# Performance work log

Measured on AMD Instinct MI355X. Metric: run time of the kernel, lower is better.

## Reference

```python
import jax, jax.numpy as jnp
import numpy as np

S = 7
B = 2
CLS = 20
N = CLS + B * 5  # 30
LAMBDA_COORD = 5.0
LAMBDA_NOOBJ = 0.5
BATCH = 16384


def setup_inputs() -> dict:
    key = jax.random.key(0)
    k1, k2, k3 = jax.random.split(key, 3)
    pred = jax.random.uniform(k1, (BATCH, S, S, N), dtype=jnp.float32)
    target = jax.random.uniform(k2, (BATCH, S, S, N), dtype=jnp.float32)
    # conf channel (index 4) must be exactly 0 or 1 -- it drives the obj/noobj masks
    obj = (jax.random.uniform(k3, (BATCH, S, S)) < 0.15).astype(jnp.float32)
    target = target.at[..., 4].set(obj)
    return {"pred": pred, "target": target}


def _iou(b1, b2):
    # b1: [M, B, 4] xyxy, b2: [M, 4] xyxy -> [M, B]
    lt = jnp.maximum(b1[..., :2], b2[:, None, :2])
    rb = jnp.minimum(b1[..., 2:], b2[:, None, 2:])
    wh = jnp.clip(rb - lt, 0.0)
    inter = wh[..., 0] * wh[..., 1]
    area1 = (b1[..., 2] - b1[..., 0]) * (b1[..., 3] - b1[..., 1])
    area2 = ((b2[:, 2] - b2[:, 0]) * (b2[:, 3] - b2[:, 1]))[:, None]
    union = area1 + area2 - inter
    return jnp.where(union > 0, inter / union, 0.0)


def reference(pred, target):
    batch = pred.shape[0]
    p = pred.reshape(-1, N)   # [M, 30], M = batch*S*S
    t = target.reshape(-1, N)
    obj = (t[:, 4] == 1).astype(pred.dtype)    # positive-cell mask
    noobj = (t[:, 4] == 0).astype(pred.dtype)  # negative-cell mask

    # faithful to source: conf_loc = arange(B)*B + 4 -> [4, 6]
    conf_loc = jnp.arange(B) * B + 4
    noobj_conf_loss = jnp.sum(noobj[:, None] * (p[:, conf_loc] - t[:, conf_loc]) ** 2)

    pb = p[:, : B * 5].reshape(-1, B, 5)  # [M, B, 5] (x, y, w, h, conf)
    tb = t[:, :5]                         # [M, 5] first target box per cell

    # xywh -> xyxy
    pb_xyxy = jnp.concatenate([pb[..., :2] - pb[..., 2:4] / 2,
                               pb[..., :2] + pb[..., 2:4] / 2], axis=-1)
    tb_xyxy = jnp.concatenate([tb[:, :2] - tb[:, 2:4] / 2,
                               tb[:, :2] + tb[:, 2:4] / 2], axis=-1)

    iou = _iou(pb_xyxy, tb_xyxy)                         # [M, B]
    j = jnp.argmax(iou, axis=1)                          # responsible box index
    max_iou = jax.lax.stop_gradient(jnp.max(iou, axis=1))
    resp = jnp.take_along_axis(pb, j[:, None, None], axis=1)[:, 0]  # [M, 5]

    xy_loss = jnp.sum((resp[:, :2] - tb[:, :2]) ** 2, axis=-1)
    wh_loss = jnp.sum((jnp.sqrt(jnp.clip(resp[:, 2:4], 0.0))
                       - jnp.sqrt(jnp.clip(tb[:, 2:4], 0.0))) ** 2, axis=-1)
    coord_loss = jnp.sum(obj * (xy_loss + wh_loss))

    obj_conf_loss = jnp.sum(obj * (resp[:, 4] - max_iou) ** 2)
    class_loss = jnp.sum(obj[:, None] * (p[:, B * 5:] - t[:, B * 5:]) ** 2)

    total = (LAMBDA_COORD * coord_loss + obj_conf_loss
             + LAMBDA_NOOBJ * noobj_conf_loss + class_loss) / batch
    return total
```

## Files before the change

kernel.cpp:

```cpp
#include <hip/hip_runtime.h>


#define TPB 256
#define NPER 30
#define R_TOTAL (16384 * 7 * 7)
#define NBLOCKS (R_TOTAL / TPB)

__global__ __launch_bounds__(TPB, 4) void yolo_loss_kernel(
    const float* __restrict__ pred, const float* __restrict__ target,
    float* __restrict__ out)
{
    __shared__ float red[TPB / 64];

    const int tid = threadIdx.x;
    const size_t cell = (size_t)blockIdx.x * TPB + tid;

    float p[NPER], t[NPER];
    {
        const float2* gp = (const float2*)(pred + cell * NPER);
        const float2* gt = (const float2*)(target + cell * NPER);
        #pragma unroll
        for (int i = 0; i < NPER / 2; i++) {
            float2 v = gp[i];
            p[2 * i] = v.x; p[2 * i + 1] = v.y;
        }
        #pragma unroll
        for (int i = 0; i < NPER / 2; i++) {
            float2 v = gt[i];
            t[2 * i] = v.x; t[2 * i + 1] = v.y;
        }
    }

    float sum = 0.0f;
    const float t4 = t[4];
    if (t4 == 0.0f) {
        float d4 = p[4] - t[4];
        float d6 = p[6] - t[6];
        sum = 0.5f * (d4 * d4 + d6 * d6);
    } else if (t4 == 1.0f) {
        float tx1 = t[0] - t[2] * 0.5f, ty1 = t[1] - t[3] * 0.5f;
        float tx2 = t[0] + t[2] * 0.5f, ty2 = t[1] + t[3] * 0.5f;
        float area2 = (tx2 - tx1) * (ty2 - ty1);

        float ax1 = p[0] - p[2] * 0.5f, ay1 = p[1] - p[3] * 0.5f;
        float ax2 = p[0] + p[2] * 0.5f, ay2 = p[1] + p[3] * 0.5f;
        float w0 = fmaxf(fminf(ax2, tx2) - fmaxf(ax1, tx1), 0.0f);
        float h0 = fmaxf(fminf(ay2, ty2) - fmaxf(ay1, ty1), 0.0f);
        float inter0 = w0 * h0;
        float uni0 = (ax2 - ax1) * (ay2 - ay1) + area2 - inter0;
        float iou0 = (uni0 > 0.0f) ? (inter0 / uni0) : 0.0f;

        float bx1 = p[5] - p[7] * 0.5f, by1 = p[6] - p[8] * 0.5f;
        float bx2 = p[5] + p[7] * 0.5f, by2 = p[6] + p[8] * 0.5f;
        float w1 = fmaxf(fminf(bx2, tx2) - fmaxf(bx1, tx1), 0.0f);
        float h1 = fmaxf(fminf(by2, ty2) - fmaxf(by1, ty1), 0.0f);
        float inter1 = w1 * h1;
        float uni1 = (bx2 - bx1) * (by2 - by1) + area2 - inter1;
        float iou1 = (uni1 > 0.0f) ? (inter1 / uni1) : 0.0f;

        bool j1 = (iou1 > iou0);
        float max_iou = fmaxf(iou0, iou1);
        float r0 = j1 ? p[5] : p[0];
        float r1 = j1 ? p[6] : p[1];
        float r2 = j1 ? p[7] : p[2];
        float r3 = j1 ? p[8] : p[3];
        float r4 = j1 ? p[9] : p[4];

        float dx = r0 - t[0];
        float dy = r1 - t[1];
        float sw = sqrtf(fmaxf(r2, 0.0f)) - sqrtf(fmaxf(t[2], 0.0f));
        float sh = sqrtf(fmaxf(r3, 0.0f)) - sqrtf(fmaxf(t[3], 0.0f));
        float coord = dx * dx + dy * dy + sw * sw + sh * sh;
        float dc = r4 - max_iou;

        float cls = 0.0f;
        #pragma unroll
        for (int k = 10; k < NPER; k++) {
            float d = p[k] - t[k];
            cls += d * d;
        }
        sum = 5.0f * coord + dc * dc + cls;
    }

    #pragma unroll
    for (int off = 32; off > 0; off >>= 1)
        sum += __shfl_down(sum, off, 64);
    if ((tid & 63) == 0) red[tid >> 6] = sum;
    __syncthreads();
    if (tid == 0) {
        float s = red[0] + red[1] + red[2] + red[3];
        atomicAdd(out, s * (1.0f / 16384.0f));
    }
}

extern "C" void kernel_launch(void* const* d_in, const int* in_sizes, int n_in,
                              void* d_out, int out_size, void* d_ws, size_t ws_size,
                              hipStream_t stream) {
    const float* pred = (const float*)d_in[0];
    const float* target = (const float*)d_in[1];
    float* out = (float*)d_out;
    hipMemsetAsync(out, 0, sizeof(float), stream);
    yolo_loss_kernel<<<NBLOCKS, TPB, 0, stream>>>(pred, target, out);
}
```

Measured before the change: 211.3 us.

## Stream cells through double-buffered LDS via direct global-to-LDS loads in persistent wavefronts

Replaces the one-thread-per-cell kernel, which makes strided float2 loads, with a persistent grid of 512 single-wavefront blocks. Each block copies 128-cell chunks of pred and target into LDS with global_load_lds 16-byte transfers, double-buffered and guarded by s_waitcnt vmcnt so the next chunk arrives while the current one is computed. Global reads become fully coalesced and per-block atomics drop to 512. In exchange, the 60 KB LDS per block limits occupancy to about two wavefronts per CU, the manual vmcnt count depends on the compiler emitting exactly 30 loads, and LDS reads at a 120-byte stride may cause bank conflicts.

```diff
diff --git a/kernel.cpp b/kernel.cpp
--- a/kernel.cpp
+++ b/kernel.cpp
@@ -1,96 +1,119 @@
 #include <hip/hip_runtime.h>
 
 
-#define TPB 256
-#define NPER 30
+#define TPB 64
+#define CPC 128
+#define CB  (CPC * 120)
+#define NCALLS (CB / 1024)
 #define R_TOTAL (16384 * 7 * 7)
-#define NBLOCKS (R_TOTAL / TPB)
+#define NCHUNKS (R_TOTAL / CPC)
+#define GRID 512
 
-__global__ __launch_bounds__(TPB, 4) void yolo_loss_kernel(
+__device__ __forceinline__ void gload_lds16(const void* g, void* l) {
+    __builtin_amdgcn_global_load_lds(
+        (const __attribute__((address_space(1))) void*)g,
+        (__attribute__((address_space(3))) void*)l, 16, 0, 0);
+}
+
+__global__ __launch_bounds__(TPB) void yolo_loss_kernel(
     const float* __restrict__ pred, const float* __restrict__ target,
     float* __restrict__ out)
 {
-    __shared__ float red[TPB / 64];
+    __shared__ __align__(16) unsigned char smem[2][2 * CB];
 
-    const int tid = threadIdx.x;
-    const size_t cell = (size_t)blockIdx.x * TPB + tid;
+    const int lane = threadIdx.x;
+    float sum = 0.0f;
 
-    float p[NPER], t[NPER];
     {
-        const float2* gp = (const float2*)(pred + cell * NPER);
-        const float2* gt = (const float2*)(target + cell * NPER);
+        const char* gp = (const char*)pred + (size_t)blockIdx.x * CB + lane * 16;
+        const char* gt = (const char*)target + (size_t)blockIdx.x * CB + lane * 16;
         #pragma unroll
-        for (int i = 0; i < NPER / 2; i++) {
-            float2 v = gp[i];
-            p[2 * i] = v.x; p[2 * i + 1] = v.y;
-        }
+        for (int c = 0; c < NCALLS; c++) gload_lds16(gp + c * 1024, &smem[0][c * 1024]);
         #pragma unroll
-        for (int i = 0; i < NPER / 2; i++) {
-            float2 v = gt[i];
-            t[2 * i] = v.x; t[2 * i + 1] = v.y;
-        }
+        for (int c = 0; c < NCALLS; c++) gload_lds16(gt + c * 1024, &smem[0][CB + c * 1024]);
     }
 
-    float sum = 0.0f;
-    const float t4 = t[4];
-    if (t4 == 0.0f) {
-        float d4 = p[4] - t[4];
-        float d6 = p[6] - t[6];
-        sum = 0.5f * (d4 * d4 + d6 * d6);
-    } else if (t4 == 1.0f) {
-        float tx1 = t[0] - t[2] * 0.5f, ty1 = t[1] - t[3] * 0.5f;
-        float tx2 = t[0] + t[2] * 0.5f, ty2 = t[1] + t[3] * 0.5f;
-        float area2 = (tx2 - tx1) * (ty2 - ty1);
+    int buf = 0;
+    for (size_t chunk = blockIdx.x; chunk < NCHUNKS; chunk += GRID) {
+        const size_t next = chunk + GRID;
+        if (next < NCHUNKS) {
+            const char* gp = (const char*)pred + next * CB + lane * 16;
+            const char* gt = (const char*)target + next * CB + lane * 16;
+            unsigned char* lb = smem[buf ^ 1];
+            #pragma unroll
+            for (int c = 0; c < NCALLS; c++) gload_lds16(gp + c * 1024, lb + c * 1024);
+            #pragma unroll
+            for (int c = 0; c < NCALLS; c++) gload_lds16(gt + c * 1024, lb + CB + c * 1024);
+            asm volatile("s_waitcnt vmcnt(30)" ::: "memory");
+        } else {
+            asm volatile("s_waitcnt vmcnt(0)" ::: "memory");
+        }
 
-        float ax1 = p[0] - p[2] * 0.5f, ay1 = p[1] - p[3] * 0.5f;
-        float ax2 = p[0] + p[2] * 0.5f, ay2 = p[1] + p[3] * 0.5f;
-        float w0 = fmaxf(fminf(ax2, tx2) - fmaxf(ax1, tx1), 0.0f);
-        float h0 = fmaxf(fminf(ay2, ty2) - fmaxf(ay1, ty1), 0.0f);
-        float inter0 = w0 * h0;
-        float uni0 = (ax2 - ax1) * (ay2 - ay1) + area2 - inter0;
-        float iou0 = (uni0 > 0.0f) ? (inter0 / uni0) : 0.0f;
+        const unsigned char* lb = smem[buf];
+        #pragma unroll
+        for (int half = 0; half < 2; half++) {
+            const int cell = lane + half * 64;
+            const float* pf = (const float*)(lb + cell * 120);
+            const float* tf = (const float*)(lb + CB + cell * 120);
 
-        float bx1 = p[5] - p[7] * 0.5f, by1 = p[6] - p[8] * 0.5f;
-        float bx2 = p[5] + p[7] * 0.5f, by2 = p[6] + p[8] * 0.5f;
-        float w1 = fmaxf(fminf(bx2, tx2) - fmaxf(bx1, tx1), 0.0f);
-        float h1 = fmaxf(fminf(by2, ty2) - fmaxf(by1, ty1), 0.0f);
-        float inter1 = w1 * h1;
-        float uni1 = (bx2 - bx1) * (by2 - by1) + area2 - inter1;
-        float iou1 = (uni1 > 0.0f) ? (inter1 / uni1) : 0.0f;
+            const float t4 = tf[4];
+            if (t4 == 0.0f) {
+                float d4 = pf[4] - t4;
+                float d6 = pf[6] - tf[6];
+                sum += 0.5f * (d4 * d4 + d6 * d6);
+            } else if (t4 == 1.0f) {
+                float tx1 = tf[0] - tf[2] * 0.5f, ty1 = tf[1] - tf[3] * 0.5f;
+                float tx2 = tf[0] + tf[2] * 0.5f, ty2 = tf[1] + tf[3] * 0.5f;
+                float area2 = (tx2 - tx1) * (ty2 - ty1);
 
-        bool j1 = (iou1 > iou0);
-        float max_iou = fmaxf(iou0, iou1);
-        float r0 = j1 ? p[5] : p[0];
-        float r1 = j1 ? p[6] : p[1];
-        float r2 = j1 ? p[7] : p[2];
-        float r3 = j1 ? p[8] : p[3];
-        float r4 = j1 ? p[9] : p[4];
+                float ax1 = pf[0] - pf[2] * 0.5f, ay1 = pf[1] - pf[3] * 0.5f;
+                float ax2 = pf[0] + pf[2] * 0.5f, ay2 = pf[1] + pf[3] * 0.5f;
+                float w0 = fmaxf(fminf(ax2, tx2) - fmaxf(ax1, tx1), 0.0f);
+                float h0 = fmaxf(fminf(ay2, ty2) - fmaxf(ay1, ty1), 0.0f);
+                float inter0 = w0 * h0;
+                float uni0 = (ax2 - ax1) * (ay2 - ay1) + area2 - inter0;
+                float iou0 = (uni0 > 0.0f) ? (inter0 / uni0) : 0.0f;
 
-        float dx = r0 - t[0];
-        float dy = r1 - t[1];
-        float sw = sqrtf(fmaxf(r2, 0.0f)) - sqrtf(fmaxf(t[2], 0.0f));
-        float sh = sqrtf(fmaxf(r3, 0.0f)) - sqrtf(fmaxf(t[3], 0.0f));
-        float coord = dx * dx + dy * dy + sw * sw + sh * sh;
-        float dc = r4 - max_iou;
+                float bx1 = pf[5] - pf[7] * 0.5f, by1 = pf[6] - pf[8] * 0.5f;
+                float bx2 = pf[5] + pf[7] * 0.5f, by2 = pf[6] + pf[8] * 0.5f;
+                float w1 = fmaxf(fminf(bx2, tx2) - fmaxf(bx1, tx1), 0.0f);
+                float h1 = fmaxf(fminf(by2, ty2) - fmaxf(by1, ty1), 0.0f);
+                float inter1 = w1 * h1;
+                float uni1 = (bx2 - bx1) * (by2 - by1) + area2 - inter1;
+                float iou1 = (uni1 > 0.0f) ? (inter1 / uni1) : 0.0f;
 
-        float cls = 0.0f;
-        #pragma unroll
-        for (int k = 10; k < NPER; k++) {
-            float d = p[k] - t[k];
-            cls += d * d;
+                bool j1 = (iou1 > iou0);
+                float max_iou = fmaxf(iou0, iou1);
+                float r0 = j1 ? pf[5] : pf[0];
+                float r1 = j1 ? pf[6] : pf[1];
+                float r2 = j1 ? pf[7] : pf[2];
+                float r3 = j1 ? pf[8] : pf[3];
+                float r4 = j1 ? pf[9] : pf[4];
+
+                float dx = r0 - tf[0];
+                float dy = r1 - tf[1];
+                float sw = sqrtf(fmaxf(r2, 0.0f)) - sqrtf(fmaxf(tf[2], 0.0f));
+                float sh = sqrtf(fmaxf(r3, 0.0f)) - sqrtf(fmaxf(tf[3], 0.0f));
+                float coord = dx * dx + dy * dy + sw * sw + sh * sh;
+                float dc = r4 - max_iou;
+
+                float cls = 0.0f;
+                #pragma unroll
+                for (int k = 10; k < 30; k++) {
+                    float d = pf[k] - tf[k];
+                    cls += d * d;
+                }
+                sum += 5.0f * coord + dc * dc + cls;
+            }
         }
-        sum = 5.0f * coord + dc * dc + cls;
+        buf ^= 1;
     }
 
     #pragma unroll
     for (int off = 32; off > 0; off >>= 1)
         sum += __shfl_down(sum, off, 64);
-    if ((tid & 63) == 0) red[tid >> 6] = sum;
-    __syncthreads();
-    if (tid == 0) {
-        float s = red[0] + red[1] + red[2] + red[3];
-        atomicAdd(out, s * (1.0f / 16384.0f));
-    }
+    if (lane == 0)
+        atomicAdd(out, sum * (1.0f / 16384.0f));
 }
 
 extern "C" void kernel_launch(void* const* d_in, const int* in_sizes, int n_in,
@@ -100,5 +123,5 @@
     const float* target = (const float*)d_in[1];
     float* out = (float*)d_out;
     hipMemsetAsync(out, 0, sizeof(float), stream);
-    yolo_loss_kernel<<<NBLOCKS, TPB, 0, stream>>>(pred, target, out);
+    yolo_loss_kernel<<<GRID, TPB, 0, stream>>>(pred, target, out);
 }
```

Result: faster. 207.0 us (-2.0%).
